# Optimization experiments

Hardware: AMD Instinct MI355X
Metric: run time of the kernel (lower is better)

## Reference

```python
import jax, jax.numpy as jnp
import numpy as np

SCALE = 0.08838834764831845  # 1/sqrt(head_dim=128)

T, H, D = 8192, 16, 128
NUM_SLOTS = 16384
SEQ_LEN = 2048


def setup_inputs() -> dict:
    key = jax.random.key(0)
    kq, kk, kv = jax.random.split(key, 3)
    q = jax.random.normal(kq, (T, H, D), dtype=jnp.float32)
    k = jax.random.normal(kk, (T, H, D), dtype=jnp.float32)
    v = jax.random.normal(kv, (T, H, D), dtype=jnp.float32)
    k_cache = jnp.zeros((NUM_SLOTS, H * D), dtype=jnp.float32)
    v_cache = jnp.zeros((NUM_SLOTS, H * D), dtype=jnp.float32)
    slot_mapping = jnp.arange(T, dtype=jnp.int32)  # contiguous slots; -1 would mean skip
    return {"q": q, "k": k, "v": v, "k_cache": k_cache, "v_cache": v_cache,
            "slot_mapping": slot_mapping, "seq_len": SEQ_LEN}


def reference(q, k, v, k_cache, v_cache, slot_mapping, seq_len):
    # --- store_kvcache: scatter per-token K/V rows into paged cache slots ---
    t, h, d = q.shape
    num_slots = k_cache.shape[0]
    # slot == -1 means "do not store"; remap to an out-of-bounds index and drop.
    safe_slots = jnp.where(slot_mapping < 0, num_slots, slot_mapping)
    k_cache = k_cache.at[safe_slots].set(k.reshape(t, h * d), mode="drop")
    v_cache = v_cache.at[safe_slots].set(v.reshape(t, h * d), mode="drop")

    # --- prefill attention reading K/V from the cache (block_tables path) ---
    # cu_seqlens = [0, S, 2S, ...]: equal-length sequences packed contiguously,
    # so the per-sequence cache slices are the first t rows reshaped to [B,S,H,D].
    b = t // seq_len
    qb = q.reshape(b, seq_len, h, d)
    kb = k_cache[:t].reshape(b, seq_len, h, d)
    vb = v_cache[:t].reshape(b, seq_len, h, d)

    scores = jnp.einsum("bqhd,bkhd->bhqk", qb, kb) * SCALE  # [B,H,S,S]
    causal = jnp.tril(jnp.ones((seq_len, seq_len), dtype=bool))
    scores = jnp.where(causal[None, None], scores, -jnp.inf)
    p = jax.nn.softmax(scores, axis=-1)
    o = jnp.einsum("bhqk,bkhd->bqhd", p, vb)
    return o.reshape(t, h, d)
```

## Files before the change

### kernel.cpp

```cpp
#include <hip/hip_runtime.h>

typedef float f32x16 __attribute__((ext_vector_type(16)));
typedef __bf16 bf16x8 __attribute__((ext_vector_type(8)));
typedef unsigned int uint2v __attribute__((ext_vector_type(2)));

#define Hh 16
#define Dd 128
#define SEQ 2048
#define HD 2048
#define ATT_C 0.12751743f
#define NEGINF (-__builtin_inff())

__device__ __forceinline__ ushort f2bf(float f) {
    uint u = __builtin_bit_cast(uint, f);
    return (ushort)((u + 0x7FFFu + ((u >> 16) & 1u)) >> 16);
}

__device__ __forceinline__ uint4 pack8(float4 a, float4 b) {
    uint4 u;
    u.x = (uint)f2bf(a.x) | ((uint)f2bf(a.y) << 16);
    u.y = (uint)f2bf(a.z) | ((uint)f2bf(a.w) << 16);
    u.z = (uint)f2bf(b.x) | ((uint)f2bf(b.y) << 16);
    u.w = (uint)f2bf(b.z) | ((uint)f2bf(b.w) << 16);
    return u;
}

__device__ __forceinline__ uint cvtpk(float a, float b) {
    uint r;
    asm("v_cvt_pk_bf16_f32 %0, %1, %2" : "=v"(r) : "v"(a), "v"(b));
    return r;
}

__device__ __forceinline__ f32x16 zero16() {
    f32x16 v;
#pragma unroll
    for (int i = 0; i < 16; ++i) v[i] = 0.f;
    return v;
}

__device__ __forceinline__ void gll16(const void* g, void* l) {
    __builtin_amdgcn_global_load_lds(
        (const __attribute__((address_space(1))) unsigned int*)g,
        (__attribute__((address_space(3))) unsigned int*)l, 16, 0, 0);
}

__device__ __forceinline__ bf16x8 mkfrag(uint a01, uint a23, uint a45, uint a67, int hi) {
    uint4 u;
#if __has_builtin(__builtin_amdgcn_permlane32_swap)
    uint2v xz = __builtin_amdgcn_permlane32_swap(a01, a45, false, false);
    uint2v yw = __builtin_amdgcn_permlane32_swap(a23, a67, false, false);
    u.x = xz[0]; u.y = yw[0]; u.z = xz[1]; u.w = yw[1];
    (void)hi;
#else
    uint s01 = __shfl_xor(a01, 32), s23 = __shfl_xor(a23, 32);
    uint s45 = __shfl_xor(a45, 32), s67 = __shfl_xor(a67, 32);
    u.x = hi ? s45 : a01;
    u.y = hi ? s67 : a23;
    u.z = hi ? a45 : s01;
    u.w = hi ? a67 : s23;
#endif
    return __builtin_bit_cast(bf16x8, u);
}

__global__ void initinv(int* __restrict__ inv, int T) {
    int i = blockIdx.x * 256 + threadIdx.x;
    if (i < T) inv[i] = -1;
}
__global__ void buildinv(const int* __restrict__ slots, int* __restrict__ inv, int T) {
    int t = blockIdx.x * 256 + threadIdx.x;
    if (t < T) { int s = slots[t]; if (s >= 0 && s < T) inv[s] = t; }
}

__global__ void fusekv(const float* __restrict__ k, const float* __restrict__ v,
                       const float* __restrict__ kc, const float* __restrict__ vc,
                       const int* __restrict__ inv, ushort* __restrict__ ek,
                       ushort* __restrict__ evt) {
    __shared__ int sv[64];
    __shared__ ushort Ks[64][136];
    __shared__ ushort Lt[128][72];
    const int tid = threadIdx.x;
    const int r0 = blockIdx.x * 64, h = blockIdx.y;
    const int b = r0 >> 11, tok0 = r0 & (SEQ - 1);
    const long tb = ((long)(b * Hh + h) * 32 + (tok0 >> 6)) * 8192;
    if (tid < 64) sv[tid] = inv[r0 + tid];
    __syncthreads();
#pragma unroll
    for (int i = 0; i < 4; ++i) {
        int idx = i * 256 + tid, r = idx >> 4, sg = idx & 15;
        int s = sv[r];
        const float* src = (s >= 0 ? k + (long)s * HD : kc + (long)(r0 + r) * HD) + h * Dd + sg * 8;
        float4 A = *(const float4*)src;
        float4 Bv = *(const float4*)(src + 4);
        *(uint4*)&Ks[r][sg * 8] = pack8(A, Bv);
    }
    const int d = tid & 127, hf2 = tid >> 7;
#pragma unroll
    for (int i = 0; i < 8; ++i) {
        const int t = i * 8 + hf2 * 4;
        ushort wv[4];
#pragma unroll
        for (int jj = 0; jj < 4; ++jj) {
            int s = sv[t + jj];
            const float* sp = (s >= 0 ? v + (long)s * HD : vc + (long)(r0 + t + jj) * HD) + h * Dd + d;
            wv[jj] = f2bf(*sp);
        }
        uint2 u;
        u.x = (uint)wv[0] | ((uint)wv[1] << 16);
        u.y = (uint)wv[2] | ((uint)wv[3] << 16);
        *(uint2*)&Lt[d][t] = u;
    }
    __syncthreads();
#pragma unroll
    for (int i = 0; i < 4; ++i) {
        int c = i * 256 + tid, l = c & 31, j = (c >> 5) & 15, hf = c >> 9;
        *(uint4*)(ek + tb + (long)c * 8) = *(const uint4*)&Ks[hf * 32 + l][j * 8];
    }
#pragma unroll
    for (int i = 0; i < 4; ++i) {
        int c = i * 256 + tid, l = c & 31, ch = (c >> 5) & 7, nt = c >> 8;
        *(uint4*)(evt + tb + (long)c * 8) = *(const uint4*)&Lt[nt * 32 + l][ch * 8];
    }
}

__global__ __launch_bounds__(512, 2) void attn32(const float* __restrict__ q,
                                                 const ushort* __restrict__ ek,
                                                 const ushort* __restrict__ evt,
                                                 float* __restrict__ out) {
    __shared__ ushort KV[2][16384];

    const int tid = threadIdx.x;
    const int w = tid >> 6, lane = tid & 63;
    const int l31 = lane & 31, hi = lane >> 5;
    const int g = blockIdx.x;
    const int bh = g & 63, jp = g >> 6;
    const int b = bh >> 4, h = bh & 15;
    const int n1 = 4 * (jp + 1), ns = 36;
    const long kvbase = (long)bh * 32 * 8192;
    const int koff = hi * 256 + l31 * 8;

    bf16x8 qf[8];
    auto loadq = [&](int qt_) {
        const int qrow = qt_ * 256 + w * 32 + l31;
        const float* qp = q + ((long)(b * SEQ + qrow) * Hh + h) * Dd + hi * 8;
#pragma unroll
        for (int kk = 0; kk < 8; ++kk) {
            float4 A = *(const float4*)(qp + kk * 16);
            float4 Bv = *(const float4*)(qp + kk * 16 + 4);
            A.x *= ATT_C; A.y *= ATT_C; A.z *= ATT_C; A.w *= ATT_C;
            Bv.x *= ATT_C; Bv.y *= ATT_C; Bv.z *= ATT_C; Bv.w *= ATT_C;
            union { uint4 u; bf16x8 v; } cv;
            cv.u = pack8(A, Bv);
            qf[kk] = cv.v;
        }
    };
    auto stage = [&](int nb, int t) {
        const ushort* kg = ek + kvbase + (long)t * 8192 + tid * 8;
        const ushort* vg = evt + kvbase + (long)t * 8192 + tid * 8;
        ushort* kl = &KV[nb][tid * 8];
        ushort* vl = &KV[nb][8192 + tid * 8];
#pragma unroll
        for (int i = 0; i < 2; ++i) {
            gll16(kg + i * 4096, kl + i * 4096);
            gll16(vg + i * 4096, vl + i * 4096);
        }
    };

    f32x16 o[4];
#pragma unroll
    for (int nt = 0; nt < 4; ++nt) o[nt] = zero16();
    float m = NEGINF, lsum = 0.f;

    stage(0, 0);
    loadq(jp);
    __syncthreads();

    int cur = 0;
    int qt = jp, qtb = qt * 256 + w * 32;

    for (int s = 0; s < ns; ++s) {
        if (s + 1 < ns) stage(cur ^ 1, (s + 1 < n1) ? s + 1 : s + 1 - n1);
        if (s == n1) { qt = 7 - jp; qtb = qt * 256 + w * 32; loadq(qt); }
        const int kv0 = ((s < n1) ? s : s - n1) * 64;
        const int qpos = qtb + l31;
        const ushort* Kb = &KV[cur][0];
        const ushort* Vb = &KV[cur][8192];

        if (kv0 <= qtb + 31) {
            const bool h2full = (kv0 + 32 <= qtb + 31);
            f32x16 s0 = zero16(), s1;
            __builtin_amdgcn_s_setprio(1);
            if (h2full) {
                s1 = zero16();
#pragma unroll
                for (int kk = 0; kk < 8; ++kk) {
                    s0 = __builtin_amdgcn_mfma_f32_32x32x16_bf16(
                        *(const bf16x8*)&Kb[kk * 512 + koff], qf[kk], s0, 0, 0, 0);
                    s1 = __builtin_amdgcn_mfma_f32_32x32x16_bf16(
                        *(const bf16x8*)&Kb[4096 + kk * 512 + koff], qf[kk], s1, 0, 0, 0);
                }
            } else {
#pragma unroll
                for (int kk = 0; kk < 8; ++kk)
                    s0 = __builtin_amdgcn_mfma_f32_32x32x16_bf16(
                        *(const bf16x8*)&Kb[kk * 512 + koff], qf[kk], s0, 0, 0, 0);
            }
            __builtin_amdgcn_s_setprio(0);

            float mt = NEGINF;
            const bool needmask = (kv0 + 63 > qtb);
            if (needmask) {
#pragma unroll
                for (int r = 0; r < 16; ++r) {
                    const int kr = kv0 + ((r & 3) + 8 * (r >> 2) + 4 * hi);
                    float a0 = (kr <= qpos) ? s0[r] : NEGINF;
                    s0[r] = a0;
                    mt = fmaxf(mt, a0);
                }
                if (h2full) {
#pragma unroll
                    for (int r = 0; r < 16; ++r) {
                        const int kr = kv0 + 32 + ((r & 3) + 8 * (r >> 2) + 4 * hi);
                        float a1 = (kr <= qpos) ? s1[r] : NEGINF;
                        s1[r] = a1;
                        mt = fmaxf(mt, a1);
                    }
                }
            } else {
#pragma unroll
                for (int r = 0; r < 16; ++r) mt = fmaxf(mt, fmaxf(s0[r], s1[r]));
            }
            mt = fmaxf(mt, __shfl_xor(mt, 32));

            if (!__all(mt <= m + 8.f)) {
                const float mn = fmaxf(m, mt);
                const float al = exp2f(m - mn);
                m = mn;
                lsum *= al;
#pragma unroll
                for (int r = 0; r < 16; ++r) {
                    const float alr = __shfl(al, (r & 3) + 8 * (r >> 2) + 4 * hi);
                    o[0][r] *= alr; o[1][r] *= alr; o[2][r] *= alr; o[3][r] *= alr;
                }
            }

            float psum = 0.f;
#pragma unroll
            for (int r = 0; r < 16; ++r) {
                s0[r] = __builtin_amdgcn_exp2f(s0[r] - m);
                psum += s0[r];
            }
            if (h2full) {
#pragma unroll
                for (int r = 0; r < 16; ++r) {
                    s1[r] = __builtin_amdgcn_exp2f(s1[r] - m);
                    psum += s1[r];
                }
            }
            lsum += psum;

            bf16x8 pa00 = mkfrag(cvtpk(s0[0], s0[1]), cvtpk(s0[2], s0[3]),
                                 cvtpk(s0[4], s0[5]), cvtpk(s0[6], s0[7]), hi);
            bf16x8 pa01 = mkfrag(cvtpk(s0[8], s0[9]), cvtpk(s0[10], s0[11]),
                                 cvtpk(s0[12], s0[13]), cvtpk(s0[14], s0[15]), hi);
            __builtin_amdgcn_s_setprio(1);
#pragma unroll
            for (int nt = 0; nt < 4; ++nt) {
                const int vb = nt * 2048 + koff;
                o[nt] = __builtin_amdgcn_mfma_f32_32x32x16_bf16(
                    pa00, *(const bf16x8*)&Vb[vb], o[nt], 0, 0, 0);
                o[nt] = __builtin_amdgcn_mfma_f32_32x32x16_bf16(
                    pa01, *(const bf16x8*)&Vb[vb + 512], o[nt], 0, 0, 0);
            }
            __builtin_amdgcn_s_setprio(0);
            if (h2full) {
                bf16x8 pa10 = mkfrag(cvtpk(s1[0], s1[1]), cvtpk(s1[2], s1[3]),
                                     cvtpk(s1[4], s1[5]), cvtpk(s1[6], s1[7]), hi);
                bf16x8 pa11 = mkfrag(cvtpk(s1[8], s1[9]), cvtpk(s1[10], s1[11]),
                                     cvtpk(s1[12], s1[13]), cvtpk(s1[14], s1[15]), hi);
                __builtin_amdgcn_s_setprio(1);
#pragma unroll
                for (int nt = 0; nt < 4; ++nt) {
                    const int vb = nt * 2048 + koff;
                    o[nt] = __builtin_amdgcn_mfma_f32_32x32x16_bf16(
                        pa10, *(const bf16x8*)&Vb[vb + 1024], o[nt], 0, 0, 0);
                    o[nt] = __builtin_amdgcn_mfma_f32_32x32x16_bf16(
                        pa11, *(const bf16x8*)&Vb[vb + 1536], o[nt], 0, 0, 0);
                }
                __builtin_amdgcn_s_setprio(0);
            }
        }

        if (s == n1 - 1 || s == ns - 1) {
            const float lt = lsum + __shfl_xor(lsum, 32);
            const float inv_ = 1.f / lt;
#pragma unroll
            for (int r = 0; r < 16; ++r) {
                const int qr = (r & 3) + 8 * (r >> 2) + 4 * hi;
                const float ivr = __shfl(inv_, qr);
                float* op = out + ((long)(b * SEQ + qtb + qr) * Hh + h) * Dd + l31;
                op[0]  = o[0][r] * ivr;
                op[32] = o[1][r] * ivr;
                op[64] = o[2][r] * ivr;
                op[96] = o[3][r] * ivr;
            }
#pragma unroll
            for (int nt = 0; nt < 4; ++nt) o[nt] = zero16();
            m = NEGINF; lsum = 0.f;
        }

        __syncthreads();
        cur ^= 1;
    }
}

extern "C" void kernel_launch(void* const* d_in, const int* in_sizes, int n_in,
                              void* d_out, int out_size, void* d_ws, size_t ws_size,
                              hipStream_t stream) {
    const float* q = (const float*)d_in[0];
    const float* k = (const float*)d_in[1];
    const float* v = (const float*)d_in[2];
    const float* k_cache = (const float*)d_in[3];
    const float* v_cache = (const float*)d_in[4];
    const int* slot_mapping = (const int*)d_in[5];
    float* out = (float*)d_out;

    const int T = in_sizes[0] / HD;
    (void)n_in; (void)out_size; (void)ws_size;

    ushort* ek = (ushort*)d_ws;
    ushort* evt = ek + (size_t)T * HD;
    int* inv = (int*)(evt + (size_t)T * HD);

    initinv<<<T / 256, 256, 0, stream>>>(inv, T);
    buildinv<<<T / 256, 256, 0, stream>>>(slot_mapping, inv, T);
    fusekv<<<dim3(T / 64, Hh), 256, 0, stream>>>(k, v, k_cache, v_cache, inv, ek, evt);
    attn32<<<dim3(256), 512, 0, stream>>>(q, ek, evt, out);
}
```

Baseline: 153.6 us.

## Software-pipeline QK of next tile with softmax/PV of current using 4-stage LDS ring

Restructures the attention loop so the QK^T MFMAs for tile s+1 are issued before the softmax and PV of tile s, letting matrix and vector work overlap across iterations. The LDS buffer grows from 2 to 4 stages, prefetching three tiles ahead with explicit vmcnt waits and raw s_barrier in place of __syncthreads. Both Q tiles are preloaded into registers, and QK is split into two independent accumulator chains per half. The cost is higher register pressure (two Q fragment sets plus two score sets) and double LDS usage, which may reduce occupancy. Partially masked half-tiles are now computed in full and masked rather than skipped.

After: 239.6 us. +56.0%, slower.

```diff
diff --git a/kernel.cpp b/kernel.cpp
--- a/kernel.cpp
+++ b/kernel.cpp
@@ -36,6 +36,21 @@
 #pragma unroll
     for (int i = 0; i < 16; ++i) v[i] = 0.f;
     return v;
+}
+
+__device__ __forceinline__ float hmax16(const f32x16 v) {
+    float a0 = fmaxf(v[0], v[1]), a1 = fmaxf(v[2], v[3]);
+    float a2 = fmaxf(v[4], v[5]), a3 = fmaxf(v[6], v[7]);
+    float a4 = fmaxf(v[8], v[9]), a5 = fmaxf(v[10], v[11]);
+    float a6 = fmaxf(v[12], v[13]), a7 = fmaxf(v[14], v[15]);
+    float b0 = fmaxf(a0, a1), b1 = fmaxf(a2, a3), b2 = fmaxf(a4, a5), b3 = fmaxf(a6, a7);
+    return fmaxf(fmaxf(b0, b1), fmaxf(b2, b3));
+}
+__device__ __forceinline__ float hsum16(const f32x16 v) {
+    float a0 = v[0] + v[1], a1 = v[2] + v[3], a2 = v[4] + v[5], a3 = v[6] + v[7];
+    float a4 = v[8] + v[9], a5 = v[10] + v[11], a6 = v[12] + v[13], a7 = v[14] + v[15];
+    float b0 = a0 + a1, b1 = a2 + a3, b2 = a4 + a5, b3 = a6 + a7;
+    return (b0 + b1) + (b2 + b3);
 }
 
 __device__ __forceinline__ void gll16(const void* g, void* l) {
@@ -122,11 +137,22 @@
     }
 }
 
+#define QKB(QF) { \
+    f32x16 a0 = zero16(), b0 = zero16(), a1 = zero16(), b1 = zero16(); \
+    _Pragma("unroll") \
+    for (int kk = 0; kk < 4; ++kk) { \
+        a0 = __builtin_amdgcn_mfma_f32_32x32x16_bf16(*(const bf16x8*)&Kb[kk * 512 + koff], QF[kk], a0, 0, 0, 0); \
+        a1 = __builtin_amdgcn_mfma_f32_32x32x16_bf16(*(const bf16x8*)&Kb[4096 + kk * 512 + koff], QF[kk], a1, 0, 0, 0); \
+        b0 = __builtin_amdgcn_mfma_f32_32x32x16_bf16(*(const bf16x8*)&Kb[(kk + 4) * 512 + koff], QF[kk + 4], b0, 0, 0, 0); \
+        b1 = __builtin_amdgcn_mfma_f32_32x32x16_bf16(*(const bf16x8*)&Kb[4096 + (kk + 4) * 512 + koff], QF[kk + 4], b1, 0, 0, 0); \
+    } \
+    zn0 = a0 + b0; zn1 = a1 + b1; }
+
 __global__ __launch_bounds__(512, 2) void attn32(const float* __restrict__ q,
                                                  const ushort* __restrict__ ek,
                                                  const ushort* __restrict__ evt,
                                                  float* __restrict__ out) {
-    __shared__ ushort KV[2][16384];
+    __shared__ ushort KV[4][16384];
 
     const int tid = threadIdx.x;
     const int w = tid >> 6, lane = tid & 63;
@@ -138,8 +164,8 @@
     const long kvbase = (long)bh * 32 * 8192;
     const int koff = hi * 256 + l31 * 8;
 
-    bf16x8 qf[8];
-    auto loadq = [&](int qt_) {
+    bf16x8 qfA[8], qfB[8];
+    auto loadq = [&](int qt_, bf16x8* qf) {
         const int qrow = qt_ * 256 + w * 32 + l31;
         const float* qp = q + ((long)(b * SEQ + qrow) * Hh + h) * Dd + hi * 8;
 #pragma unroll
@@ -170,69 +196,67 @@
     for (int nt = 0; nt < 4; ++nt) o[nt] = zero16();
     float m = NEGINF, lsum = 0.f;
 
-    stage(0, 0);
-    loadq(jp);
-    __syncthreads();
-
-    int cur = 0;
-    int qt = jp, qtb = qt * 256 + w * 32;
-
-    for (int s = 0; s < ns; ++s) {
-        if (s + 1 < ns) stage(cur ^ 1, (s + 1 < n1) ? s + 1 : s + 1 - n1);
-        if (s == n1) { qt = 7 - jp; qtb = qt * 256 + w * 32; loadq(qt); }
-        const int kv0 = ((s < n1) ? s : s - n1) * 64;
-        const int qpos = qtb + l31;
-        const ushort* Kb = &KV[cur][0];
-        const ushort* Vb = &KV[cur][8192];
-
-        if (kv0 <= qtb + 31) {
-            const bool h2full = (kv0 + 32 <= qtb + 31);
-            f32x16 s0 = zero16(), s1;
+    auto masknext = [&](int kv0n, int qtbn, f32x16& zn0, f32x16& zn1) -> float {
+        float mm = NEGINF;
+        if (kv0n + 63 > qtbn) {
+            const int qpn = qtbn + l31;
+#pragma unroll
+            for (int r = 0; r < 16; ++r) {
+                const int kr = kv0n + ((r & 3) + 8 * (r >> 2) + 4 * hi);
+                float a0 = (kr <= qpn) ? zn0[r] : NEGINF;
+                float a1 = (kr + 32 <= qpn) ? zn1[r] : NEGINF;
+                zn0[r] = a0; zn1[r] = a1;
+                mm = fmaxf(mm, fmaxf(a0, a1));
+            }
+        } else {
+            mm = fmaxf(hmax16(zn0), hmax16(zn1));
+        }
+        return fmaxf(mm, __shfl_xor(mm, 32));
+    };
+
+    loadq(jp, qfA);
+    loadq(7 - jp, qfB);
+    stage(0, 0); stage(1, 1); stage(2, 2);
+    asm volatile("s_waitcnt vmcnt(8)" ::: "memory");
+    __builtin_amdgcn_sched_barrier(0);
+    __builtin_amdgcn_s_barrier();
+
+    f32x16 zA0, zA1, zB0, zB1;
+    float mA = NEGINF, mB = NEGINF;
+    {
+        const ushort* Kb = &KV[0][0];
+        f32x16& zn0 = zA0; f32x16& zn1 = zA1;
+        QKB(qfA);
+        mA = masknext(0, jp * 256 + w * 32, zA0, zA1);
+    }
+    asm volatile("s_waitcnt vmcnt(4)" ::: "memory");
+    __builtin_amdgcn_sched_barrier(0);
+    __builtin_amdgcn_s_barrier();
+
+    auto body = [&](int s, f32x16& zc0, f32x16& zc1, float& mtc,
+                    f32x16& zn0_, f32x16& zn1_, float& mtn) {
+        const int kv0c = ((s < n1) ? s : s - n1) * 64;
+        const int qtbc = ((s < n1) ? jp : 7 - jp) * 256 + w * 32;
+        const bool liveC = (kv0c <= qtbc + 31);
+        const int sp1 = s + 1;
+        const bool haveN = (sp1 < ns);
+        const int kv0n = haveN ? (((sp1 < n1) ? sp1 : sp1 - n1) * 64) : 0;
+        const int qtbn = ((sp1 < n1) ? jp : 7 - jp) * 256 + w * 32;
+        const bool liveN = haveN && (kv0n <= qtbn + 31);
+
+        if (s + 3 < ns) stage((s + 3) & 3, (s + 3 < n1) ? s + 3 : s + 3 - n1);
+
+        if (liveN) {
+            const ushort* Kb = &KV[sp1 & 3][0];
+            f32x16& zn0 = zn0_; f32x16& zn1 = zn1_;
             __builtin_amdgcn_s_setprio(1);
-            if (h2full) {
-                s1 = zero16();
-#pragma unroll
-                for (int kk = 0; kk < 8; ++kk) {
-                    s0 = __builtin_amdgcn_mfma_f32_32x32x16_bf16(
-                        *(const bf16x8*)&Kb[kk * 512 + koff], qf[kk], s0, 0, 0, 0);
-                    s1 = __builtin_amdgcn_mfma_f32_32x32x16_bf16(
-                        *(const bf16x8*)&Kb[4096 + kk * 512 + koff], qf[kk], s1, 0, 0, 0);
-                }
-            } else {
-#pragma unroll
-                for (int kk = 0; kk < 8; ++kk)
-                    s0 = __builtin_amdgcn_mfma_f32_32x32x16_bf16(
-                        *(const bf16x8*)&Kb[kk * 512 + koff], qf[kk], s0, 0, 0, 0);
-            }
+            if (sp1 < n1) { QKB(qfA) } else { QKB(qfB) }
             __builtin_amdgcn_s_setprio(0);
-
-            float mt = NEGINF;
-            const bool needmask = (kv0 + 63 > qtb);
-            if (needmask) {
-#pragma unroll
-                for (int r = 0; r < 16; ++r) {
-                    const int kr = kv0 + ((r & 3) + 8 * (r >> 2) + 4 * hi);
-                    float a0 = (kr <= qpos) ? s0[r] : NEGINF;
-                    s0[r] = a0;
-                    mt = fmaxf(mt, a0);
-                }
-                if (h2full) {
-#pragma unroll
-                    for (int r = 0; r < 16; ++r) {
-                        const int kr = kv0 + 32 + ((r & 3) + 8 * (r >> 2) + 4 * hi);
-                        float a1 = (kr <= qpos) ? s1[r] : NEGINF;
-                        s1[r] = a1;
-                        mt = fmaxf(mt, a1);
-                    }
-                }
-            } else {
-#pragma unroll
-                for (int r = 0; r < 16; ++r) mt = fmaxf(mt, fmaxf(s0[r], s1[r]));
-            }
-            mt = fmaxf(mt, __shfl_xor(mt, 32));
-
-            if (!__all(mt <= m + 8.f)) {
-                const float mn = fmaxf(m, mt);
+        }
+
+        if (liveC) {
+            if (!__all(mtc <= m + 8.f)) {
+                const float mn = fmaxf(m, mtc);
                 const float al = exp2f(m - mn);
                 m = mn;
                 lsum *= al;
@@ -242,53 +266,34 @@
                     o[0][r] *= alr; o[1][r] *= alr; o[2][r] *= alr; o[3][r] *= alr;
                 }
             }
-
-            float psum = 0.f;
 #pragma unroll
             for (int r = 0; r < 16; ++r) {
-                s0[r] = __builtin_amdgcn_exp2f(s0[r] - m);
-                psum += s0[r];
-            }
-            if (h2full) {
-#pragma unroll
-                for (int r = 0; r < 16; ++r) {
-                    s1[r] = __builtin_amdgcn_exp2f(s1[r] - m);
-                    psum += s1[r];
-                }
-            }
-            lsum += psum;
-
-            bf16x8 pa00 = mkfrag(cvtpk(s0[0], s0[1]), cvtpk(s0[2], s0[3]),
-                                 cvtpk(s0[4], s0[5]), cvtpk(s0[6], s0[7]), hi);
-            bf16x8 pa01 = mkfrag(cvtpk(s0[8], s0[9]), cvtpk(s0[10], s0[11]),
-                                 cvtpk(s0[12], s0[13]), cvtpk(s0[14], s0[15]), hi);
+                zc0[r] = __builtin_amdgcn_exp2f(zc0[r] - m);
+                zc1[r] = __builtin_amdgcn_exp2f(zc1[r] - m);
+            }
+            lsum += hsum16(zc0) + hsum16(zc1);
+            bf16x8 pa0 = mkfrag(cvtpk(zc0[0], zc0[1]), cvtpk(zc0[2], zc0[3]),
+                                cvtpk(zc0[4], zc0[5]), cvtpk(zc0[6], zc0[7]), hi);
+            bf16x8 pa1 = mkfrag(cvtpk(zc0[8], zc0[9]), cvtpk(zc0[10], zc0[11]),
+                                cvtpk(zc0[12], zc0[13]), cvtpk(zc0[14], zc0[15]), hi);
+            bf16x8 pa2 = mkfrag(cvtpk(zc1[0], zc1[1]), cvtpk(zc1[2], zc1[3]),
+                                cvtpk(zc1[4], zc1[5]), cvtpk(zc1[6], zc1[7]), hi);
+            bf16x8 pa3 = mkfrag(cvtpk(zc1[8], zc1[9]), cvtpk(zc1[10], zc1[11]),
+                                cvtpk(zc1[12], zc1[13]), cvtpk(zc1[14], zc1[15]), hi);
+            const ushort* Vb = &KV[s & 3][8192];
             __builtin_amdgcn_s_setprio(1);
 #pragma unroll
             for (int nt = 0; nt < 4; ++nt) {
                 const int vb = nt * 2048 + koff;
-                o[nt] = __builtin_amdgcn_mfma_f32_32x32x16_bf16(
-                    pa00, *(const bf16x8*)&Vb[vb], o[nt], 0, 0, 0);
-                o[nt] = __builtin_amdgcn_mfma_f32_32x32x16_bf16(
-                    pa01, *(const bf16x8*)&Vb[vb + 512], o[nt], 0, 0, 0);
+                o[nt] = __builtin_amdgcn_mfma_f32_32x32x16_bf16(pa0, *(const bf16x8*)&Vb[vb], o[nt], 0, 0, 0);
+                o[nt] = __builtin_amdgcn_mfma_f32_32x32x16_bf16(pa1, *(const bf16x8*)&Vb[vb + 512], o[nt], 0, 0, 0);
+                o[nt] = __builtin_amdgcn_mfma_f32_32x32x16_bf16(pa2, *(const bf16x8*)&Vb[vb + 1024], o[nt], 0, 0, 0);
+                o[nt] = __builtin_amdgcn_mfma_f32_32x32x16_bf16(pa3, *(const bf16x8*)&Vb[vb + 1536], o[nt], 0, 0, 0);
             }
             __builtin_amdgcn_s_setprio(0);
-            if (h2full) {
-                bf16x8 pa10 = mkfrag(cvtpk(s1[0], s1[1]), cvtpk(s1[2], s1[3]),
-                                     cvtpk(s1[4], s1[5]), cvtpk(s1[6], s1[7]), hi);
-                bf16x8 pa11 = mkfrag(cvtpk(s1[8], s1[9]), cvtpk(s1[10], s1[11]),
-                                     cvtpk(s1[12], s1[13]), cvtpk(s1[14], s1[15]), hi);
-                __builtin_amdgcn_s_setprio(1);
-#pragma unroll
-                for (int nt = 0; nt < 4; ++nt) {
-                    const int vb = nt * 2048 + koff;
-                    o[nt] = __builtin_amdgcn_mfma_f32_32x32x16_bf16(
-                        pa10, *(const bf16x8*)&Vb[vb + 1024], o[nt], 0, 0, 0);
-                    o[nt] = __builtin_amdgcn_mfma_f32_32x32x16_bf16(
-                        pa11, *(const bf16x8*)&Vb[vb + 1536], o[nt], 0, 0, 0);
-                }
-                __builtin_amdgcn_s_setprio(0);
-            }
-        }
+        }
+
+        if (liveN) mtn = masknext(kv0n, qtbn, zn0_, zn1_);
 
         if (s == n1 - 1 || s == ns - 1) {
             const float lt = lsum + __shfl_xor(lsum, 32);
@@ -297,8 +302,8 @@
             for (int r = 0; r < 16; ++r) {
                 const int qr = (r & 3) + 8 * (r >> 2) + 4 * hi;
                 const float ivr = __shfl(inv_, qr);
-                float* op = out + ((long)(b * SEQ + qtb + qr) * Hh + h) * Dd + l31;
-                op[0]  = o[0][r] * ivr;
+                float* op = out + ((long)(b * SEQ + qtbc + qr) * Hh + h) * Dd + l31;
+                op[0] = o[0][r] * ivr;
                 op[32] = o[1][r] * ivr;
                 op[64] = o[2][r] * ivr;
                 op[96] = o[3][r] * ivr;
@@ -308,8 +313,15 @@
             m = NEGINF; lsum = 0.f;
         }
 
-        __syncthreads();
-        cur ^= 1;
+        if (s + 2 < ns) { asm volatile("s_waitcnt vmcnt(4)" ::: "memory"); }
+        else            { asm volatile("s_waitcnt vmcnt(0)" ::: "memory"); }
+        __builtin_amdgcn_sched_barrier(0);
+        __builtin_amdgcn_s_barrier();
+    };
+
+    for (int s = 0; s < ns; s += 2) {
+        body(s,     zA0, zA1, mA, zB0, zB1, mB);
+        body(s + 1, zB0, zB1, mB, zA0, zA1, mA);
     }
 }
 
```
